# Optimization experiments

Hardware: AMD Instinct MI355X
Metric: run time of the kernel (lower is better)

The kernel has to match this reference:

```python
import jax, jax.numpy as jnp
import numpy as np

VOCAB, EMBED, ENC, DEC, ATT = 10000, 256, 2048, 512, 512
B, P, T = 64, 49, 30


def setup_inputs() -> dict:
    key = jax.random.key(0)
    ks = jax.random.split(key, 20)
    s = 0.02
    emb = jax.random.normal(ks[0], (VOCAB, EMBED), jnp.float32) * s
    emb = emb.at[0].set(0.0)  # padding_idx=0
    inp = {
        'features': jax.random.normal(ks[1], (B, P, ENC), jnp.float32),
        'captions': jax.random.randint(ks[2], (B, T), 0, VOCAB),
        'emb': emb,
        'W1': jax.random.normal(ks[3], (ATT, ENC), jnp.float32) * s,
        'b1': jnp.zeros((ATT,), jnp.float32),
        'W2': jax.random.normal(ks[4], (ATT, DEC), jnp.float32) * s,
        'b2': jnp.zeros((ATT,), jnp.float32),
        'V': jax.random.normal(ks[5], (1, ATT), jnp.float32) * s,
        'bV': jnp.zeros((1,), jnp.float32),
        'W_ih1': jax.random.normal(ks[6], (4 * DEC, EMBED + ENC), jnp.float32) * s,
        'W_hh1': jax.random.normal(ks[7], (4 * DEC, DEC), jnp.float32) * s,
        'b_ih1': jnp.zeros((4 * DEC,), jnp.float32),
        'b_hh1': jnp.zeros((4 * DEC,), jnp.float32),
        'W_ih2': jax.random.normal(ks[8], (4 * DEC, DEC), jnp.float32) * s,
        'W_hh2': jax.random.normal(ks[9], (4 * DEC, DEC), jnp.float32) * s,
        'b_ih2': jnp.zeros((4 * DEC,), jnp.float32),
        'b_hh2': jnp.zeros((4 * DEC,), jnp.float32),
        'fc_W': jax.random.normal(ks[10], (VOCAB, DEC), jnp.float32) * s,
        'fc_b': jnp.zeros((VOCAB,), jnp.float32),
    }
    return inp


def _lstm_cell(x, h, c, Wih, Whh, bih, bhh):
    g = x @ Wih.T + bih + h @ Whh.T + bhh  # [B, 4D]
    i, f, gg, o = jnp.split(g, 4, axis=-1)  # PyTorch gate order i,f,g,o
    c_new = jax.nn.sigmoid(f) * c + jax.nn.sigmoid(i) * jnp.tanh(gg)
    h_new = jax.nn.sigmoid(o) * jnp.tanh(c_new)
    return h_new, c_new


def reference(features, captions, emb, W1, b1, W2, b2, V, bV,
              W_ih1, W_hh1, b_ih1, b_hh1, W_ih2, W_hh2, b_ih2, b_hh2,
              fc_W, fc_b):
    # dropout is identity (eval mode / deterministic reference)
    batch = features.shape[0]
    dec = W_hh1.shape[1]
    feat_W1 = jnp.einsum('bpe,ae->bpa', features, W1) + b1  # precompute W1(features)
    embs = emb[captions]  # [B, T, E]

    def step(carry, x_t):
        h1, c1, h2, c2 = carry
        # Bahdanau attention with hidden state h2
        att = jnp.tanh(feat_W1 + (h2 @ W2.T + b2)[:, None, :])  # [B, P, A]
        score = att @ V.T + bV  # [B, P, 1]
        w = jax.nn.softmax(score, axis=1)
        ctx = jnp.sum(w * features, axis=1)  # [B, ENC]
        lstm_in = jnp.concatenate([x_t, ctx], axis=1)
        h1n, c1n = _lstm_cell(lstm_in, h1, c1, W_ih1, W_hh1, b_ih1, b_hh1)
        h2n, c2n = _lstm_cell(h1n, h2, c2, W_ih2, W_hh2, b_ih2, b_hh2)
        out = h2n @ fc_W.T + fc_b  # [B, V]
        return (h1n, c1n, h2n, c2n), out

    init = tuple(jnp.zeros((batch, dec), features.dtype) for _ in range(4))
    _, outs = jax.lax.scan(step, init, jnp.swapaxes(embs, 0, 1))  # [T, B, V]
    return jnp.swapaxes(outs, 0, 1)  # [B, T, V]
```

## Files before the change

kernel.cpp:

```cpp
#include <hip/hip_runtime.h>
#include <math.h>

#define VOCAB 10000
#define VPAD  10240
#define EMBED 256
#define ENC   2048
#define DEC   512
#define ATT   512
#define B_    64
#define P_    49
#define T_    30
#define G4    2048
#define SL    32768

typedef __bf16 bf16_t;
typedef bf16_t bf16x8 __attribute__((ext_vector_type(8)));
typedef float  f32x4  __attribute__((ext_vector_type(4)));

__device__ __forceinline__ float sigf(float x) { return 1.f / (1.f + expf(-x)); }

__global__ void prep_k(
    const float* __restrict__ b_ih1, const float* __restrict__ b_hh1, float* __restrict__ bsum1,
    const float* __restrict__ b_ih2, const float* __restrict__ b_hh2, float* __restrict__ bsum2,
    const float* __restrict__ W2,    bf16_t* __restrict__ W2sp,
    const float* __restrict__ W_hh1, bf16_t* __restrict__ fp1h,
    const float* __restrict__ W_ih2, const float* __restrict__ W_hh2, bf16_t* __restrict__ fp2,
    const float* __restrict__ fc_W,  bf16_t* __restrict__ fcWb,
    const float* __restrict__ features, bf16_t* __restrict__ featb,
    const int* __restrict__ caps, const float* __restrict__ emb, bf16_t* __restrict__ xgb,
    bf16_t* __restrict__ h1s0, bf16_t* __restrict__ h2s0,
    float* __restrict__ c1s0, float* __restrict__ c2s0,
    float* __restrict__ hwp, float* __restrict__ G1h)
{
    long stride = (long)gridDim.x * blockDim.x;
    long i0 = (long)blockIdx.x * blockDim.x + threadIdx.x;
    for (long i = i0; i < SL; i += stride) {
        h1s0[i] = (bf16_t)0.f; h2s0[i] = (bf16_t)0.f;
        c1s0[i] = 0.f; c2s0[i] = 0.f;
    }
    for (long i = i0; i < 32L * SL; i += stride) hwp[i] = 0.f;
    for (long i = i0; i < 64L * 2048; i += stride) G1h[i] = 0.f;
    for (long i = i0; i < 2048; i += stride) {
        bsum1[i] = b_ih1[i] + b_hh1[i];
        bsum2[i] = b_ih2[i] + b_hh2[i];
    }
    for (long i = i0; i < 32L * 32 * 64 * 8; i += stride) {
        long j8 = i & 7, lq = (i >> 3) & 63, nt = (i >> 9) & 31, nb = i >> 14;
        long k = (lq >> 4) * 8 + j8;
        long a = nt * 16 + (lq & 15);
        W2sp[i] = (bf16_t)(k < 16 ? W2[a * 512 + nb * 16 + k] : 0.f);
    }
    for (long i = i0; i < 32L * 16 * 2048; i += stride) {
        long j8 = i & 7, lq = (i >> 3) & 63, s = (i >> 9) & 3, nk = i >> 11;
        long kf = nk & 15, nb = nk >> 4;
        long c = s * 512 + nb * 16 + (lq & 15);
        long k = kf * 32 + (lq >> 4) * 8 + j8;
        fp1h[i] = (bf16_t)W_hh1[c * 512 + k];
    }
    for (long i = i0; i < 2048L * 1024; i += stride) {
        long j8 = i & 7, lq = (i >> 3) & 63, s = (i >> 9) & 3, nk = i >> 11;
        long kf = nk & 31, nb = nk >> 5;
        long c = s * 512 + nb * 16 + (lq & 15);
        long k = kf * 32 + (lq >> 4) * 8 + j8;
        fp2[i] = (bf16_t)(k < 512 ? W_ih2[c * 512 + k] : W_hh2[c * 512 + (k - 512)]);
    }
    for (long i = i0; i < (long)VPAD * 512; i += stride) {
        long r = i >> 9;
        fcWb[i] = (bf16_t)(r < VOCAB ? fc_W[i] : 0.f);
    }
    for (long i = i0; i < 3136L * 2048; i += stride) featb[i] = (bf16_t)features[i];
    for (long i = i0; i < 1920L * 256; i += stride) {
        long row = i >> 8, e = i & 255;
        long tq = row >> 6, b = row & 63;
        int cap = caps[b * T_ + tq];
        xgb[i] = (bf16_t)emb[(long)cap * 256 + e];
    }
}

__global__ __launch_bounds__(256) void mm_f32b(
    const bf16_t* __restrict__ A, int lda,
    const float* __restrict__ Bw, int ldb, int boff,
    const float* __restrict__ bias,
    bf16_t* __restrict__ outB, int ldo, int K)
{
    __shared__ bf16_t Apad[64][72];
    __shared__ bf16_t Bpad[64][72];
    const int bn = blockIdx.x * 64, bm = blockIdx.y * 64;
    const int tid = threadIdx.x;
    const int w = tid >> 6, l = tid & 63;
    f32x4 acc[4] = {};

    for (int k0 = 0; k0 < K; k0 += 64) {
        for (int c = tid; c < 512; c += 256) {
            int row = c >> 3, q = c & 7;
            *(bf16x8*)&Apad[row][q * 8] = *(const bf16x8*)&A[(size_t)(bm + row) * lda + k0 + q * 8];
            const float* bs = &Bw[(size_t)(bn + row) * ldb + boff + k0 + q * 8];
            float4 f0 = *(const float4*)bs;
            float4 f1 = *(const float4*)(bs + 4);
            bf16x8 v;
            v[0] = (bf16_t)f0.x; v[1] = (bf16_t)f0.y; v[2] = (bf16_t)f0.z; v[3] = (bf16_t)f0.w;
            v[4] = (bf16_t)f1.x; v[5] = (bf16_t)f1.y; v[6] = (bf16_t)f1.z; v[7] = (bf16_t)f1.w;
            *(bf16x8*)&Bpad[row][q * 8] = v;
        }
        __syncthreads();
#pragma unroll
        for (int ks = 0; ks < 2; ++ks) {
            bf16x8 a8 = *(const bf16x8*)&Apad[w * 16 + (l & 15)][ks * 32 + (l >> 4) * 8];
#pragma unroll
            for (int nf = 0; nf < 4; ++nf) {
                bf16x8 b8 = *(const bf16x8*)&Bpad[nf * 16 + (l & 15)][ks * 32 + (l >> 4) * 8];
                acc[nf] = __builtin_amdgcn_mfma_f32_16x16x32_bf16(a8, b8, acc[nf], 0, 0, 0);
            }
        }
        __syncthreads();
    }

    int rbase = bm + w * 16 + (l >> 4) * 4;
    int cl = l & 15;
#pragma unroll
    for (int nf = 0; nf < 4; ++nf) {
        int col = bn + nf * 16 + cl;
        float bv = bias ? bias[col] : 0.f;
#pragma unroll
        for (int j = 0; j < 4; ++j)
            outB[(size_t)(rbase + j) * ldo + col] = (bf16_t)(acc[nf][j] + bv);
    }
}

__global__ __launch_bounds__(256) void mm_fc(
    const bf16_t* __restrict__ A, int lda,
    const bf16_t* __restrict__ Bw, int ldb,
    const float* __restrict__ bias,
    float* __restrict__ outF, int ldo, int N, int K)
{
    __shared__ bf16_t Apad[64][72];
    __shared__ bf16_t Bpad[64][72];
    const int bn = blockIdx.x * 64, bm = blockIdx.y * 64;
    const int tid = threadIdx.x;
    const int w = tid >> 6, l = tid & 63;
    f32x4 acc[4] = {};

    for (int k0 = 0; k0 < K; k0 += 64) {
        for (int c = tid; c < 512; c += 256) {
            int row = c >> 3, q = c & 7;
            *(bf16x8*)&Apad[row][q * 8] = *(const bf16x8*)&A[(size_t)(bm + row) * lda + k0 + q * 8];
            *(bf16x8*)&Bpad[row][q * 8] = *(const bf16x8*)&Bw[(size_t)(bn + row) * ldb + k0 + q * 8];
        }
        __syncthreads();
#pragma unroll
        for (int ks = 0; ks < 2; ++ks) {
            bf16x8 a8 = *(const bf16x8*)&Apad[w * 16 + (l & 15)][ks * 32 + (l >> 4) * 8];
#pragma unroll
            for (int nf = 0; nf < 4; ++nf) {
                bf16x8 b8 = *(const bf16x8*)&Bpad[nf * 16 + (l & 15)][ks * 32 + (l >> 4) * 8];
                acc[nf] = __builtin_amdgcn_mfma_f32_16x16x32_bf16(a8, b8, acc[nf], 0, 0, 0);
            }
        }
        __syncthreads();
    }

    int rbase = bm + w * 16 + (l >> 4) * 4;
    int cl = l & 15;
#pragma unroll
    for (int nf = 0; nf < 4; ++nf) {
        int col = bn + nf * 16 + cl;
#pragma unroll
        for (int j = 0; j < 4; ++j) {
            int row = rbase + j;
            if (col < N) {
                int orow = (row & 63) * T_ + (row >> 6);
                outF[(size_t)orow * ldo + col] = acc[nf][j] + bias[col];
            }
        }
    }
}

__global__ __launch_bounds__(256) void attn1_k(
    const float* __restrict__ hwp, const float* __restrict__ b2,
    const bf16_t* __restrict__ fW1b, const float* __restrict__ V,
    const float* __restrict__ bV, const bf16_t* __restrict__ F1g,
    const bf16_t* __restrict__ xeb, const float* __restrict__ G1h,
    const float* __restrict__ c1r, float* __restrict__ c1w,
    bf16_t* __restrict__ h1w)
{
    const int b = blockIdx.x, tid = threadIdx.x;
    const int w = tid >> 6, l = tid & 63;
    __shared__ float hw[512];
    __shared__ float sc[64];
    __shared__ float wn[64];
    __shared__ float gsum[2048];

    {
        float a0 = b2[2 * tid], a1 = b2[2 * tid + 1];
        const float* hp = hwp + (size_t)b * 16384 + 2 * tid;
#pragma unroll 8
        for (int nb = 0; nb < 32; ++nb) {
            float2 v = *(const float2*)&hp[nb * 512];
            a0 += v.x; a1 += v.y;
        }
        hw[2 * tid] = a0; hw[2 * tid + 1] = a1;
    }
    __syncthreads();
    {
        float hwr[8], Vr[8];
#pragma unroll
        for (int i = 0; i < 8; ++i) { hwr[i] = hw[l * 8 + i]; Vr[i] = V[l * 8 + i]; }
        for (int pq = w; pq < P_; pq += 4) {
            bf16x8 f8 = *(const bf16x8*)&fW1b[(size_t)(b * P_ + pq) * 512 + l * 8];
            float s = 0.f;
#pragma unroll
            for (int i = 0; i < 8; ++i) s += tanhf((float)f8[i] + hwr[i]) * Vr[i];
#pragma unroll
            for (int o = 32; o; o >>= 1) s += __shfl_xor(s, o);
            if (l == 0) sc[pq] = s + bV[0];
        }
    }
    __syncthreads();
    {
        float m = -1e30f;
        for (int q = 0; q < P_; ++q) m = fmaxf(m, sc[q]);
        float ss = 0.f;
        for (int q = 0; q < P_; ++q) ss += expf(sc[q] - m);
        if (tid < P_) wn[tid] = expf(sc[tid] - m) / ss;
    }
    __syncthreads();
    {
        float acc[8] = {};
        const bf16_t* fg = F1g + (size_t)b * P_ * 2048 + tid * 8;
#pragma unroll 7
        for (int q = 0; q < P_; ++q) {
            bf16x8 f8 = *(const bf16x8*)&fg[(size_t)q * 2048];
            float wq = wn[q];
#pragma unroll
            for (int i = 0; i < 8; ++i) acc[i] += wq * (float)f8[i];
        }
#pragma unroll
        for (int i = 0; i < 8; ++i) gsum[tid * 8 + i] = acc[i];
    }
    __syncthreads();
    {
        const bf16_t* xb = xeb + (size_t)b * G4;
        const float* gh = G1h + b * 2048;
#pragma unroll
        for (int u = 0; u < 2; ++u) {
            int d = 2 * tid + u;
            float gi = (float)xb[d]        + gsum[d]        + gh[d];
            float gf = (float)xb[512 + d]  + gsum[512 + d]  + gh[512 + d];
            float gg = (float)xb[1024 + d] + gsum[1024 + d] + gh[1024 + d];
            float go = (float)xb[1536 + d] + gsum[1536 + d] + gh[1536 + d];
            int idx = b * 512 + d;
            float cn = sigf(gf) * c1r[idx] + sigf(gi) * tanhf(gg);
            c1w[idx] = cn;
            h1w[idx] = (bf16_t)(sigf(go) * tanhf(cn));
        }
    }
}

__global__ __launch_bounds__(512) void gate2_k(
    const bf16_t* __restrict__ h1n, const bf16_t* __restrict__ h2r,
    const bf16_t* __restrict__ fp2, const bf16_t* __restrict__ fp1h,
    const bf16_t* __restrict__ W2sp, const float* __restrict__ bsum2,
    const float* __restrict__ c2r, float* __restrict__ c2w,
    bf16_t* __restrict__ h2w, float* __restrict__ G1h, float* __restrict__ hwp)
{
    const int bid = blockIdx.x, tid = threadIdx.x;
    const int w = tid >> 6, l = tid & 63;
    const int l15 = l & 15, koff = (l >> 4) * 8;
    const int mt = w & 3, kh = w >> 2;
    __shared__ float red[2][4][4][256];
    __shared__ bf16_t h2t[64 * 16];

    if (bid < 32) {
        const int nb = bid;
        {
            const int arow = mt * 16 + l15;
            const bf16_t* ap = (kh == 0 ? h1n : h2r) + arow * 512 + koff;
            const bf16_t* wp = fp2 + ((size_t)nb * 32 + kh * 16) * 2048 + l * 8;
            f32x4 acc[4] = {};
#pragma unroll
            for (int kf = 0; kf < 16; ++kf) {
                bf16x8 a8 = *(const bf16x8*)&ap[kf * 32];
                const bf16_t* wk = wp + (size_t)kf * 2048;
#pragma unroll
                for (int s = 0; s < 4; ++s) {
                    bf16x8 w8 = *(const bf16x8*)&wk[s * 512];
                    acc[s] = __builtin_amdgcn_mfma_f32_16x16x32_bf16(a8, w8, acc[s], 0, 0, 0);
                }
            }
#pragma unroll
            for (int s = 0; s < 4; ++s) *(f32x4*)&red[kh][mt][s][l * 4] = acc[s];
        }
        __syncthreads();
        if (w < 4) {
            const int d = nb * 16 + l15;
            const int rb = w * 16 + ((l >> 4) << 2);
            f32x4 v[4];
#pragma unroll
            for (int s = 0; s < 4; ++s)
                v[s] = *(const f32x4*)&red[0][w][s][l * 4] + *(const f32x4*)&red[1][w][s][l * 4];
#pragma unroll
            for (int j = 0; j < 4; ++j) {
                int row = rb + j;
                float gi = v[0][j] + bsum2[d];
                float gf = v[1][j] + bsum2[512 + d];
                float gg = v[2][j] + bsum2[1024 + d];
                float go = v[3][j] + bsum2[1536 + d];
                float cn = sigf(gf) * c2r[row * 512 + d] + sigf(gi) * tanhf(gg);
                c2w[row * 512 + d] = cn;
                bf16_t hb = (bf16_t)(sigf(go) * tanhf(cn));
                h2w[row * 512 + d] = hb;
                h2t[row * 16 + l15] = hb;
            }
        }
        __syncthreads();
        {
            bf16x8 a8 = {};
            if ((l >> 4) < 2) a8 = *(const bf16x8*)&h2t[(mt * 16 + l15) * 16 + koff];
            const int row0 = mt * 16 + (l >> 4) * 4;
            for (int q = 0; q < 16; ++q) {
                int nt = kh * 16 + q;
                bf16x8 b8 = *(const bf16x8*)&W2sp[((size_t)(nb * 32 + nt) * 64 + l) * 8];
                f32x4 acc2 = {};
                acc2 = __builtin_amdgcn_mfma_f32_16x16x32_bf16(a8, b8, acc2, 0, 0, 0);
                const int col = nt * 16 + l15;
#pragma unroll
                for (int j = 0; j < 4; ++j)
                    hwp[(size_t)(row0 + j) * 16384 + nb * 512 + col] = acc2[j];
            }
        }
    } else {
        const int nb = bid - 32;
        {
            const int arow = mt * 16 + l15;
            const bf16_t* ap = h1n + arow * 512 + kh * 256 + koff;
            const bf16_t* wp = fp1h + ((size_t)nb * 16 + kh * 8) * 2048 + l * 8;
            f32x4 acc[4] = {};
#pragma unroll
            for (int kf = 0; kf < 8; ++kf) {
                bf16x8 a8 = *(const bf16x8*)&ap[kf * 32];
                const bf16_t* wk = wp + (size_t)kf * 2048;
#pragma unroll
                for (int s = 0; s < 4; ++s) {
                    bf16x8 w8 = *(const bf16x8*)&wk[s * 512];
                    acc[s] = __builtin_amdgcn_mfma_f32_16x16x32_bf16(a8, w8, acc[s], 0, 0, 0);
                }
            }
#pragma unroll
            for (int s = 0; s < 4; ++s) *(f32x4*)&red[kh][mt][s][l * 4] = acc[s];
        }
        __syncthreads();
        if (w < 4) {
            const int d = nb * 16 + l15;
            const int rb = w * 16 + ((l >> 4) << 2);
#pragma unroll
            for (int s = 0; s < 4; ++s) {
                f32x4 v = *(const f32x4*)&red[0][w][s][l * 4] + *(const f32x4*)&red[1][w][s][l * 4];
#pragma unroll
                for (int j = 0; j < 4; ++j)
                    G1h[(rb + j) * 2048 + s * 512 + d] = v[j];
            }
        }
    }
}

extern "C" void kernel_launch(void* const* d_in, const int* in_sizes, int n_in,
                              void* d_out, int out_size, void* d_ws, size_t ws_size,
                              hipStream_t stream)
{
    const float* features = (const float*)d_in[0];
    const int*   captions = (const int*)d_in[1];
    const float* emb   = (const float*)d_in[2];
    const float* W1    = (const float*)d_in[3];
    const float* b1    = (const float*)d_in[4];
    const float* W2    = (const float*)d_in[5];
    const float* b2    = (const float*)d_in[6];
    const float* V     = (const float*)d_in[7];
    const float* bV    = (const float*)d_in[8];
    const float* W_ih1 = (const float*)d_in[9];
    const float* W_hh1 = (const float*)d_in[10];
    const float* b_ih1 = (const float*)d_in[11];
    const float* b_hh1 = (const float*)d_in[12];
    const float* W_ih2 = (const float*)d_in[13];
    const float* W_hh2 = (const float*)d_in[14];
    const float* b_ih2 = (const float*)d_in[15];
    const float* b_hh2 = (const float*)d_in[16];
    const float* fc_W  = (const float*)d_in[17];
    const float* fc_b  = (const float*)d_in[18];
    float* out = (float*)d_out;

    char* ws = (char*)d_ws;
    size_t off = 0;
    auto alloc = [&](size_t nbytes) {
        char* pp = ws + off;
        off = (off + nbytes + 255) & ~(size_t)255;
        return pp;
    };
    bf16_t* featb  = (bf16_t*)alloc(3136L * 2048 * 2);
    bf16_t* fW1b   = (bf16_t*)alloc(3136L * 512 * 2);
    bf16_t* F1g    = (bf16_t*)alloc(3136L * 2048 * 2);
    bf16_t* W2sp   = (bf16_t*)alloc(32L * 32 * 64 * 8 * 2);
    bf16_t* fp1h   = (bf16_t*)alloc(32L * 16 * 2048 * 2);
    bf16_t* fp2    = (bf16_t*)alloc(2048L * 1024 * 2);
    bf16_t* fcWb   = (bf16_t*)alloc((size_t)VPAD * 512 * 2);
    bf16_t* xgb    = (bf16_t*)alloc(1920L * 256 * 2);
    bf16_t* xembb  = (bf16_t*)alloc(1920L * 2048 * 2);
    float*  bsum1  = (float*)alloc(2048 * 4);
    float*  bsum2  = (float*)alloc(2048 * 4);
    float*  hwp    = (float*)alloc(32L * SL * 4);
    float*  G1h    = (float*)alloc(64L * 2048 * 4);
    bf16_t* h1s    = (bf16_t*)alloc((size_t)(T_ + 1) * SL * 2);
    bf16_t* h2s    = (bf16_t*)alloc((size_t)(T_ + 1) * SL * 2);
    float*  c1s    = (float*)alloc(2L * SL * 4);
    float*  c2s    = (float*)alloc(2L * SL * 4);

    prep_k<<<4096, 256, 0, stream>>>(
        b_ih1, b_hh1, bsum1, b_ih2, b_hh2, bsum2,
        W2, W2sp, W_hh1, fp1h, W_ih2, W_hh2, fp2, fc_W, fcWb,
        features, featb, captions, emb, xgb,
        h1s, h2s, c1s, c2s, hwp, G1h);

    mm_f32b<<<dim3(ATT / 64, 3136 / 64), 256, 0, stream>>>(
        featb, ENC, W1, ENC, 0, b1, fW1b, ATT, ENC);
    mm_f32b<<<dim3(G4 / 64, (T_ * B_) / 64), 256, 0, stream>>>(
        xgb, EMBED, W_ih1, EMBED + ENC, 0, bsum1, xembb, G4, EMBED);
    mm_f32b<<<dim3(G4 / 64, 3136 / 64), 256, 0, stream>>>(
        featb, ENC, W_ih1, EMBED + ENC, EMBED, nullptr, F1g, G4, ENC);

    for (int t = 0; t < T_; ++t) {
        attn1_k<<<B_, 256, 0, stream>>>(
            hwp, b2, fW1b, V, bV, F1g,
            xembb + (size_t)t * B_ * G4, G1h,
            c1s + (size_t)(t & 1) * SL, c1s + (size_t)((t + 1) & 1) * SL,
            h1s + (size_t)(t + 1) * SL);
        gate2_k<<<64, 512, 0, stream>>>(
            h1s + (size_t)(t + 1) * SL, h2s + (size_t)t * SL,
            fp2, fp1h, W2sp, bsum2,
            c2s + (size_t)(t & 1) * SL, c2s + (size_t)((t + 1) & 1) * SL,
            h2s + (size_t)(t + 1) * SL, G1h, hwp);
    }

    mm_fc<<<dim3(VPAD / 64, (T_ * B_) / 64), 256, 0, stream>>>(
        h2s + SL, DEC, fcWb, DEC, fc_b, out, VOCAB, VOCAB, DEC);
}
```

Measured before the change: 1.392 ms.

## Fuse three precompute GEMMs into one launch and widen attention kernel to 512 threads

The three setup GEMMs (features·W1, embeddings·W_ih1, features·W_ih1) are merged into a single kernel that dispatches on block index. It converts fp32 features to bf16 while loading tiles, so the separate featb conversion pass and its buffer are gone. The per-step attention/LSTM1 kernel now uses 512 threads: the 49 context positions are split between two halves with a shared reduction, and each thread handles one gate column. This trades extra feature reads and conversions inside the GEMM tiles for fewer launches and a shorter serial critical path per time step.

Measured after the change: 1.140 ms. 18.1% less time.

```diff
diff --git a/kernel.cpp b/kernel.cpp
--- a/kernel.cpp
+++ b/kernel.cpp
@@ -26,7 +26,6 @@
     const float* __restrict__ W_hh1, bf16_t* __restrict__ fp1h,
     const float* __restrict__ W_ih2, const float* __restrict__ W_hh2, bf16_t* __restrict__ fp2,
     const float* __restrict__ fc_W,  bf16_t* __restrict__ fcWb,
-    const float* __restrict__ features, bf16_t* __restrict__ featb,
     const int* __restrict__ caps, const float* __restrict__ emb, bf16_t* __restrict__ xgb,
     bf16_t* __restrict__ h1s0, bf16_t* __restrict__ h2s0,
     float* __restrict__ c1s0, float* __restrict__ c2s0,
@@ -68,7 +67,6 @@
         long r = i >> 9;
         fcWb[i] = (bf16_t)(r < VOCAB ? fc_W[i] : 0.f);
     }
-    for (long i = i0; i < 3136L * 2048; i += stride) featb[i] = (bf16_t)features[i];
     for (long i = i0; i < 1920L * 256; i += stride) {
         long row = i >> 8, e = i & 255;
         long tq = row >> 6, b = row & 63;
@@ -77,15 +75,34 @@
     }
 }
 
-__global__ __launch_bounds__(256) void mm_f32b(
-    const bf16_t* __restrict__ A, int lda,
-    const float* __restrict__ Bw, int ldb, int boff,
-    const float* __restrict__ bias,
-    bf16_t* __restrict__ outB, int ldo, int K)
-{
+__global__ __launch_bounds__(256) void mm3_k(
+    const float* __restrict__ features, const bf16_t* __restrict__ xgb,
+    const float* __restrict__ W1, const float* __restrict__ W_ih1,
+    const float* __restrict__ b1, const float* __restrict__ bsum1,
+    bf16_t* __restrict__ fW1b, bf16_t* __restrict__ xembb, bf16_t* __restrict__ F1g)
+{
+    int bid = blockIdx.x;
+    const float* Af; const bf16_t* Ab = nullptr; int lda;
+    const float* Bw; int ldb, boff;
+    const float* bias; bf16_t* outB; int ldo, K, bn, bm;
+    if (bid < 392) {
+        Af = features; lda = ENC; Bw = W1; ldb = ENC; boff = 0;
+        bias = b1; outB = fW1b; ldo = ATT; K = ENC;
+        bn = (bid & 7) * 64; bm = (bid >> 3) * 64;
+    } else if (bid < 1352) {
+        int b2i = bid - 392;
+        Af = nullptr; Ab = xgb; lda = EMBED; Bw = W_ih1; ldb = EMBED + ENC; boff = 0;
+        bias = bsum1; outB = xembb; ldo = G4; K = EMBED;
+        bn = (b2i & 31) * 64; bm = (b2i >> 5) * 64;
+    } else {
+        int b3i = bid - 1352;
+        Af = features; lda = ENC; Bw = W_ih1; ldb = EMBED + ENC; boff = EMBED;
+        bias = nullptr; outB = F1g; ldo = G4; K = ENC;
+        bn = (b3i & 31) * 64; bm = (b3i >> 5) * 64;
+    }
+
     __shared__ bf16_t Apad[64][72];
     __shared__ bf16_t Bpad[64][72];
-    const int bn = blockIdx.x * 64, bm = blockIdx.y * 64;
     const int tid = threadIdx.x;
     const int w = tid >> 6, l = tid & 63;
     f32x4 acc[4] = {};
@@ -93,7 +110,17 @@
     for (int k0 = 0; k0 < K; k0 += 64) {
         for (int c = tid; c < 512; c += 256) {
             int row = c >> 3, q = c & 7;
-            *(bf16x8*)&Apad[row][q * 8] = *(const bf16x8*)&A[(size_t)(bm + row) * lda + k0 + q * 8];
+            if (Af) {
+                const float* as = &Af[(size_t)(bm + row) * lda + k0 + q * 8];
+                float4 f0 = *(const float4*)as;
+                float4 f1 = *(const float4*)(as + 4);
+                bf16x8 v;
+                v[0] = (bf16_t)f0.x; v[1] = (bf16_t)f0.y; v[2] = (bf16_t)f0.z; v[3] = (bf16_t)f0.w;
+                v[4] = (bf16_t)f1.x; v[5] = (bf16_t)f1.y; v[6] = (bf16_t)f1.z; v[7] = (bf16_t)f1.w;
+                *(bf16x8*)&Apad[row][q * 8] = v;
+            } else {
+                *(bf16x8*)&Apad[row][q * 8] = *(const bf16x8*)&Ab[(size_t)(bm + row) * lda + k0 + q * 8];
+            }
             const float* bs = &Bw[(size_t)(bn + row) * ldb + boff + k0 + q * 8];
             float4 f0 = *(const float4*)bs;
             float4 f1 = *(const float4*)(bs + 4);
@@ -175,7 +202,7 @@
     }
 }
 
-__global__ __launch_bounds__(256) void attn1_k(
+__global__ __launch_bounds__(512) void attn1_k(
     const float* __restrict__ hwp, const float* __restrict__ b2,
     const bf16_t* __restrict__ fW1b, const float* __restrict__ V,
     const float* __restrict__ bV, const bf16_t* __restrict__ F1g,
@@ -188,24 +215,21 @@
     __shared__ float hw[512];
     __shared__ float sc[64];
     __shared__ float wn[64];
-    __shared__ float gsum[2048];
+    __shared__ float gsum[2][2048];
 
     {
-        float a0 = b2[2 * tid], a1 = b2[2 * tid + 1];
-        const float* hp = hwp + (size_t)b * 16384 + 2 * tid;
+        float a0 = b2[tid];
+        const float* hp = hwp + (size_t)b * 16384 + tid;
 #pragma unroll 8
-        for (int nb = 0; nb < 32; ++nb) {
-            float2 v = *(const float2*)&hp[nb * 512];
-            a0 += v.x; a1 += v.y;
-        }
-        hw[2 * tid] = a0; hw[2 * tid + 1] = a1;
+        for (int nb = 0; nb < 32; ++nb) a0 += hp[nb * 512];
+        hw[tid] = a0;
     }
     __syncthreads();
     {
         float hwr[8], Vr[8];
 #pragma unroll
         for (int i = 0; i < 8; ++i) { hwr[i] = hw[l * 8 + i]; Vr[i] = V[l * 8 + i]; }
-        for (int pq = w; pq < P_; pq += 4) {
+        for (int pq = w; pq < P_; pq += 8) {
             bf16x8 f8 = *(const bf16x8*)&fW1b[(size_t)(b * P_ + pq) * 512 + l * 8];
             float s = 0.f;
 #pragma unroll
@@ -225,34 +249,32 @@
     }
     __syncthreads();
     {
+        const int h = tid >> 8, th = tid & 255;
+        const int p0 = h ? 25 : 0, pn = h ? 24 : 25;
         float acc[8] = {};
-        const bf16_t* fg = F1g + (size_t)b * P_ * 2048 + tid * 8;
-#pragma unroll 7
-        for (int q = 0; q < P_; ++q) {
+        const bf16_t* fg = F1g + ((size_t)b * P_ + p0) * 2048 + th * 8;
+        for (int q = 0; q < pn; ++q) {
             bf16x8 f8 = *(const bf16x8*)&fg[(size_t)q * 2048];
-            float wq = wn[q];
+            float wq = wn[p0 + q];
 #pragma unroll
             for (int i = 0; i < 8; ++i) acc[i] += wq * (float)f8[i];
         }
 #pragma unroll
-        for (int i = 0; i < 8; ++i) gsum[tid * 8 + i] = acc[i];
+        for (int i = 0; i < 8; ++i) gsum[h][th * 8 + i] = acc[i];
     }
     __syncthreads();
     {
+        const int d = tid;
         const bf16_t* xb = xeb + (size_t)b * G4;
         const float* gh = G1h + b * 2048;
-#pragma unroll
-        for (int u = 0; u < 2; ++u) {
-            int d = 2 * tid + u;
-            float gi = (float)xb[d]        + gsum[d]        + gh[d];
-            float gf = (float)xb[512 + d]  + gsum[512 + d]  + gh[512 + d];
-            float gg = (float)xb[1024 + d] + gsum[1024 + d] + gh[1024 + d];
-            float go = (float)xb[1536 + d] + gsum[1536 + d] + gh[1536 + d];
-            int idx = b * 512 + d;
-            float cn = sigf(gf) * c1r[idx] + sigf(gi) * tanhf(gg);
-            c1w[idx] = cn;
-            h1w[idx] = (bf16_t)(sigf(go) * tanhf(cn));
-        }
+        float gi = (float)xb[d]        + gsum[0][d]        + gsum[1][d]        + gh[d];
+        float gf = (float)xb[512 + d]  + gsum[0][512 + d]  + gsum[1][512 + d]  + gh[512 + d];
+        float gg = (float)xb[1024 + d] + gsum[0][1024 + d] + gsum[1][1024 + d] + gh[1024 + d];
+        float go = (float)xb[1536 + d] + gsum[0][1536 + d] + gsum[1][1536 + d] + gh[1536 + d];
+        int idx = b * 512 + d;
+        float cn = sigf(gf) * c1r[idx] + sigf(gi) * tanhf(gg);
+        c1w[idx] = cn;
+        h1w[idx] = (bf16_t)(sigf(go) * tanhf(cn));
     }
 }
 
@@ -395,7 +417,6 @@
         off = (off + nbytes + 255) & ~(size_t)255;
         return pp;
     };
-    bf16_t* featb  = (bf16_t*)alloc(3136L * 2048 * 2);
     bf16_t* fW1b   = (bf16_t*)alloc(3136L * 512 * 2);
     bf16_t* F1g    = (bf16_t*)alloc(3136L * 2048 * 2);
     bf16_t* W2sp   = (bf16_t*)alloc(32L * 32 * 64 * 8 * 2);
@@ -416,18 +437,14 @@
     prep_k<<<4096, 256, 0, stream>>>(
         b_ih1, b_hh1, bsum1, b_ih2, b_hh2, bsum2,
         W2, W2sp, W_hh1, fp1h, W_ih2, W_hh2, fp2, fc_W, fcWb,
-        features, featb, captions, emb, xgb,
+        captions, emb, xgb,
         h1s, h2s, c1s, c2s, hwp, G1h);
 
-    mm_f32b<<<dim3(ATT / 64, 3136 / 64), 256, 0, stream>>>(
-        featb, ENC, W1, ENC, 0, b1, fW1b, ATT, ENC);
-    mm_f32b<<<dim3(G4 / 64, (T_ * B_) / 64), 256, 0, stream>>>(
-        xgb, EMBED, W_ih1, EMBED + ENC, 0, bsum1, xembb, G4, EMBED);
-    mm_f32b<<<dim3(G4 / 64, 3136 / 64), 256, 0, stream>>>(
-        featb, ENC, W_ih1, EMBED + ENC, EMBED, nullptr, F1g, G4, ENC);
+    mm3_k<<<2920, 256, 0, stream>>>(
+        features, xgb, W1, W_ih1, b1, bsum1, fW1b, xembb, F1g);
 
     for (int t = 0; t < T_; ++t) {
-        attn1_k<<<B_, 256, 0, stream>>>(
+        attn1_k<<<B_, 512, 0, stream>>>(
             hwp, b2, fW1b, V, bV, F1g,
             xembb + (size_t)t * B_ * G4, G1h,
             c1s + (size_t)(t & 1) * SL, c1s + (size_t)((t + 1) & 1) * SL,
```
